# Kernel tuning notes

Hardware: AMD Instinct MI355X
Metric: run time of the kernel (lower is better)

The kernel has to match this reference:

```python
import jax, jax.numpy as jnp
import numpy as np
from jax import lax

B, C, H, W = 16, 256, 64, 64
HID = 128
EQ = 256


def _lstm_dir(x, Wih, Whh, b, hidden):
    # x: [N, T, D]; PyTorch gate order i, f, g, o
    N = x.shape[0]
    h0 = jnp.zeros((N, hidden), x.dtype)
    c0 = jnp.zeros((N, hidden), x.dtype)
    xT = jnp.swapaxes(x, 0, 1)  # [T, N, D]
    pre = jnp.einsum('tnd,gd->tng', xT, Wih) + b  # precompute input projection

    def step(carry, xt):
        h, c = carry
        g = xt + h @ Whh.T
        i, f, gg, o = jnp.split(g, 4, axis=-1)
        c = jax.nn.sigmoid(f) * c + jax.nn.sigmoid(i) * jnp.tanh(gg)
        h = jax.nn.sigmoid(o) * jnp.tanh(c)
        return (h, c), h

    _, hs = lax.scan(step, (h0, c0), pre)
    return jnp.swapaxes(hs, 0, 1)  # [N, T, hidden]


def _bilstm(x, Wih_f, Whh_f, b_f, Wih_b, Whh_b, b_b, hidden):
    hf = _lstm_dir(x, Wih_f, Whh_f, b_f, hidden)
    hb = _lstm_dir(x[:, ::-1], Wih_b, Whh_b, b_b, hidden)[:, ::-1]
    return jnp.concatenate([hf, hb], axis=-1)


def setup_inputs() -> dict:
    key = jax.random.key(0)
    ks = jax.random.split(key, 16)
    s = 1.0 / np.sqrt(HID)
    d = {}
    d['input'] = jax.random.normal(ks[0], (B, C, H, W), jnp.float32)
    # horizontal LSTM (input_size=C)
    d['h_Wih_f'] = jax.random.uniform(ks[1], (4 * HID, C), jnp.float32, -s, s)
    d['h_Whh_f'] = jax.random.uniform(ks[2], (4 * HID, HID), jnp.float32, -s, s)
    d['h_b_f'] = jax.random.uniform(ks[3], (4 * HID,), jnp.float32, -s, s)
    d['h_Wih_b'] = jax.random.uniform(ks[4], (4 * HID, C), jnp.float32, -s, s)
    d['h_Whh_b'] = jax.random.uniform(ks[5], (4 * HID, HID), jnp.float32, -s, s)
    d['h_b_b'] = jax.random.uniform(ks[6], (4 * HID,), jnp.float32, -s, s)
    # vertical LSTM (input_size=2*HID)
    d['v_Wih_f'] = jax.random.uniform(ks[7], (4 * HID, 2 * HID), jnp.float32, -s, s)
    d['v_Whh_f'] = jax.random.uniform(ks[8], (4 * HID, HID), jnp.float32, -s, s)
    d['v_b_f'] = jax.random.uniform(ks[9], (4 * HID,), jnp.float32, -s, s)
    d['v_Wih_b'] = jax.random.uniform(ks[10], (4 * HID, 2 * HID), jnp.float32, -s, s)
    d['v_Whh_b'] = jax.random.uniform(ks[11], (4 * HID, HID), jnp.float32, -s, s)
    d['v_b_b'] = jax.random.uniform(ks[12], (4 * HID,), jnp.float32, -s, s)
    # 1x1 convs (no bias)
    d['Wr'] = jax.random.normal(ks[13], (EQ, 2 * HID), jnp.float32) * 0.05
    d['Wl'] = jax.random.normal(ks[14], (EQ, C), jnp.float32) * 0.05
    d['alpha'] = jnp.zeros((1,), jnp.float32) + 0.5  # nonzero so output depends on attention
    return d


def reference(input, h_Wih_f, h_Whh_f, h_b_f, h_Wih_b, h_Whh_b, h_b_b,
              v_Wih_f, v_Whh_f, v_b_f, v_Wih_b, v_Whh_b, v_b_b, Wr, Wl, alpha):
    b, c, h, w = input.shape
    # transpose(1,3): [B, W, H, C]; horizontal LSTM runs over H for each w
    x = jnp.transpose(input, (0, 3, 2, 1))  # [B, W, H, C]
    xh = x.reshape(b * w, h, c)
    hor = _bilstm(xh, h_Wih_f, h_Whh_f, h_b_f, h_Wih_b, h_Whh_b, h_b_b, HID)
    hor = hor.reshape(b, w, h, 2 * HID)  # == torch horizontal_feature
    # vertical LSTM: sequences over W for each h-index
    xv = jnp.transpose(hor, (0, 2, 1, 3)).reshape(b * h, w, 2 * HID)
    ver = _bilstm(xv, v_Wih_f, v_Whh_f, v_b_f, v_Wih_b, v_Whh_b, v_b_b, HID)
    ver = ver.reshape(b, h, w, 2 * HID)  # vf[b, hi, wi, :]
    # torch: stack dim=2 -> [B, W, H, 2Hd]; permute(0,3,1,2) -> [B, 2Hd, W, H]
    vf = jnp.transpose(ver, (0, 3, 2, 1))  # [B, 2Hd, W, H]
    vf = jnp.einsum('oc,bcwh->bowh', Wr, vf)  # conv_right 1x1
    vf = vf.reshape(b, EQ, h * w)
    vf = jax.nn.softmax(vf, axis=2)
    # left branch
    q = jnp.einsum('oc,bchw->bohw', Wl, input)
    q_avg = jnp.mean(q, axis=(2, 3)).reshape(b, 1, EQ)
    q_avg = jax.nn.softmax(q_avg, axis=2)
    attention = jnp.matmul(q_avg, vf).reshape(b, 1, h, w)
    attention = jax.nn.sigmoid(attention)
    out = input * attention
    return out * alpha + input
```

## Files before the change

### kernel.cpp

```cpp
#include <hip/hip_runtime.h>
#include <hip/hip_bf16.h>

typedef unsigned short u16;
typedef unsigned int u32;
typedef unsigned char u8;
typedef __attribute__((ext_vector_type(8))) short s8v;
typedef __attribute__((ext_vector_type(4))) float f4v;

__device__ __forceinline__ float b2f(u16 u) {
  union { u32 i; float f; } v; v.i = ((u32)u) << 16; return v.f;
}
__device__ __forceinline__ u16 f2b(float f) {
  union { float f; u32 i; } v; v.f = f;
  u32 r = v.i + 0x7FFFu + ((v.i >> 16) & 1u);
  return (u16)(r >> 16);
}
__device__ __forceinline__ float rcpf(float x) { return __builtin_amdgcn_rcpf(x); }
__device__ __forceinline__ float ex2(float x) {
#if __has_builtin(__builtin_amdgcn_exp2f)
  return __builtin_amdgcn_exp2f(x);
#else
  return exp2f(x);
#endif
}
__device__ __forceinline__ float sigf(float x) { return rcpf(1.0f + __expf(-x)); }
template<bool HI>
__device__ __forceinline__ u32 pkfp8(float a, float b, u32 old) {
  return (u32)__builtin_amdgcn_cvt_pk_fp8_f32(a, b, (int)old, HI);
}

#define GS_IFO 1.4426950408889634f
#define GS_G   2.8853900817779268f

__device__ __forceinline__ void gl_lds16(const void* g, void* l) {
  __builtin_amdgcn_global_load_lds(
      (const __attribute__((address_space(1))) u32*)g,
      (__attribute__((address_space(3))) u32*)l, 16, 0, 0);
}

struct CvtArgs {
  const float* src[9];
  void* dst[9];
  int n4[9];
  int scl[9];
  int sh[9];
  int to8[9];
};
__global__ __launch_bounds__(256) void k_cvt(CvtArgs a) {
  int seg = blockIdx.y;
  int i = blockIdx.x * 256 + threadIdx.x;
  if (i >= a.n4[seg]) return;
  float4 v = ((const float4*)a.src[seg])[i];
  if (a.scl[seg]) {
    float s;
    if (a.scl[seg] == 2) {
      s = GS_IFO;
    } else {
      int r = i >> a.sh[seg];
      s = (((r >> 7) & 3) == 2) ? GS_G : GS_IFO;
    }
    v.x *= s; v.y *= s; v.z *= s; v.w *= s;
  }
  if (a.to8[seg]) {
    u32 p = pkfp8<false>(v.x, v.y, 0);
    p = pkfp8<true>(v.z, v.w, p);
    ((u32*)a.dst[seg])[i] = p;
  } else {
    ushort4 o;
    o.x = f2b(v.x); o.y = f2b(v.y); o.z = f2b(v.z); o.w = f2b(v.w);
    ((ushort4*)a.dst[seg])[i] = o;
  }
}

__global__ __launch_bounds__(256) void k_tin(const float* __restrict__ in,
                                             u8* __restrict__ A8,
                                             float* __restrict__ meansum) {
  int b = blockIdx.z, h = blockIdx.y, c0 = blockIdx.x * 64;
  int t = threadIdx.x, lane = t & 63, q = t >> 6;
  __shared__ u8 lT[64][68];
  const float* src = in + ((b * 256 + c0) * 64 + h) * 64;
#pragma unroll 4
  for (int i = 0; i < 16; ++i) {
    int cl = q * 16 + i;
    float v = src[cl * 4096 + lane];
    lT[cl][lane] = (u8)(pkfp8<false>(v, v, 0) & 0xffu);
    float s = v;
#pragma unroll
    for (int off = 32; off; off >>= 1) s += __shfl_xor(s, off);
    if (lane == 0) atomicAdd(&meansum[b * 256 + c0 + cl], s);
  }
  __syncthreads();
  u8* dst = A8 + (b * 4096 + h) * 256 + c0;
#pragma unroll 4
  for (int i = 0; i < 16; ++i) {
    int w = q * 16 + i;
    dst[w * 16384 + lane] = lT[lane][w];
  }
}

__global__ __launch_bounds__(256) void k_qavg(const float* __restrict__ meansum,
                                              const float* __restrict__ Wl,
                                              float* __restrict__ qavg) {
  int b = blockIdx.x, t = threadIdx.x;
  __shared__ float mean[256];
  __shared__ float red[256];
  mean[t] = meansum[b * 256 + t] * (1.0f / 4096.0f);
  __syncthreads();
  const float* wr = Wl + t * 256;
  float acc = 0.0f;
  for (int c = 0; c < 256; ++c) acc = fmaf(wr[c], mean[c], acc);
  red[t] = acc; __syncthreads();
  for (int s = 128; s; s >>= 1) { if (t < s) red[t] = fmaxf(red[t], red[t + s]); __syncthreads(); }
  float mx = red[0]; __syncthreads();
  float e = __expf(acc - mx);
  red[t] = e; __syncthreads();
  for (int s = 128; s; s >>= 1) { if (t < s) red[t] += red[t + s]; __syncthreads(); }
  qavg[b * 256 + t] = e / red[0];
}

__global__ __launch_bounds__(256, 4) void k_gemm2(const u16* __restrict__ A,
                                                  const u16* __restrict__ W,
                                                  u16* __restrict__ out, int nstride, int NT,
                                                  float* __restrict__ Zsum) {
  int nwg = gridDim.x;
  int q = nwg >> 3;
  int bid = blockIdx.x;
  int swz = (bid & 7) * q + (bid >> 3);
  int mt = swz / NT, nt = swz % NT;
  int mb = mt << 7, nb = nt << 7;
  int t = threadIdx.x, lane = t & 63, wid = t >> 6;
  int laneg = lane & 15, lk = lane >> 4;
  __shared__ __align__(16) u16 lA[128][64];
  __shared__ __align__(16) u16 lW[128][64];
  f4v acc[4][4] = {};
  int wm = wid >> 1, wn = wid & 1;
  for (int kb = 0; kb < 4; ++kb) {
    if (kb) __syncthreads();
#pragma unroll
    for (int k = 0; k < 4; ++k) {
      int rb = (wid << 5) + (k << 3);
      int r = rb + (lane >> 3);
      int cs = (lane & 7) ^ (r & 7);
      const u16* ga = A + (mb + r) * 256 + (kb << 6) + (cs << 3);
      const u16* gw = W + (nb + r) * 256 + (kb << 6) + (cs << 3);
      gl_lds16(ga, &lA[rb][0]);
      gl_lds16(gw, &lW[rb][0]);
    }
    __syncthreads();
#pragma unroll
    for (int kk = 0; kk < 2; ++kk) {
      s8v af[4], bf[4];
#pragma unroll
      for (int m = 0; m < 4; ++m) {
        int r = (wm << 6) + (m << 4) + laneg;
        int c = ((kk << 2) + lk) ^ (r & 7);
        af[m] = *(const s8v*)&lA[r][c << 3];
      }
#pragma unroll
      for (int n = 0; n < 4; ++n) {
        int r = (wn << 6) + (n << 4) + laneg;
        int c = ((kk << 2) + lk) ^ (r & 7);
        bf[n] = *(const s8v*)&lW[r][c << 3];
      }
#pragma unroll
      for (int m = 0; m < 4; ++m)
#pragma unroll
        for (int n = 0; n < 4; ++n)
          acc[m][n] = __builtin_amdgcn_mfma_f32_16x16x32_bf16(af[m], bf[n], acc[m][n], 0, 0, 0);
    }
  }
#pragma unroll
  for (int n = 0; n < 4; ++n) {
    int col = nb + (wn << 6) + (n << 4) + laneg;
    float csum = 0.f;
#pragma unroll
    for (int m = 0; m < 4; ++m) {
      int row0 = mb + (wm << 6) + (m << 4) + (lk << 2);
#pragma unroll
      for (int j = 0; j < 4; ++j) {
        float e = ex2(acc[m][n][j]);
        csum += e;
        out[(row0 + j) * nstride + col] = f2b(e);
      }
    }
    csum += __shfl_xor(csum, 16);
    csum += __shfl_xor(csum, 32);
    if (lk == 0) atomicAdd(&Zsum[((mb >> 12) << 8) + col], csum);
  }
}

template<bool OUT8>
__global__ __launch_bounds__(512, 1) void k_recur_f(const u8* __restrict__ X8,
                                                    const u8* __restrict__ Wi8,
                                                    const u16* __restrict__ Whh,
                                                    const float* __restrict__ bias_f,
                                                    const float* __restrict__ bias_b,
                                                    void* __restrict__ outp) {
  int dir = blockIdx.y;
  int s0 = blockIdx.x << 4;
  int t = threadIdx.x, lane = t & 63, w = t >> 6;
  int laneg = lane & 15, lk = lane >> 4;
  const u16* Wd = Whh + dir * 65536;
  const u8* Wi = Wi8 + dir * 131072;
  const float* bia = dir ? bias_b : bias_f;
  int hc = w << 4;
  s8v bfr[4][4];
#pragma unroll
  for (int g = 0; g < 4; ++g)
#pragma unroll
    for (int kk = 0; kk < 4; ++kk)
      bfr[g][kk] = *(const s8v*)(Wd + (g * 128 + hc + laneg) * 128 + kk * 32 + lk * 8);
  long long ifr[4][8];
#pragma unroll
  for (int g = 0; g < 4; ++g)
#pragma unroll
    for (int kk = 0; kk < 8; ++kk)
      ifr[g][kk] = *(const long long*)(Wi + (g * 128 + hc + laneg) * 256 + kk * 32 + lk * 8);
  float bval[4];
#pragma unroll
  for (int g = 0; g < 4; ++g)
    bval[g] = bia[g * 128 + hc + laneg] * ((g == 2) ? GS_G : GS_IFO);

  __shared__ __align__(16) u16 hb[2][16][136];
  __shared__ __align__(16) u8 xb[3][16][256];
  for (int i = t; i < 2 * 16 * 136; i += 512) ((u16*)hb)[i] = 0;

  float cs[4] = {0.f, 0.f, 0.f, 0.f};
  int tc0 = dir ? 63 : 0;
  int dstep = dir ? -1 : 1;
  int srw = (w << 2) + (lane >> 4);
  int c16 = lane & 15;
  const u8* xsrc = X8 + (s0 + srw) * 16384 + ((c16 ^ (srw & 7)) << 4);
  int srow = (w << 1) + (lane >> 5);
  int schunk = lane & 31;
  int rowb = ((s0 >> 6) << 12) + (s0 & 63);
  if (w < 4) {
    gl_lds16(xsrc + tc0 * 256, &xb[0][w << 2][0]);
    gl_lds16(xsrc + ((tc0 + dstep) & 63) * 256, &xb[1][w << 2][0]);
  }
  __syncthreads();
  int cur = 0;
  for (int st = 0; st < 64; ++st) {
    int tc = tc0 + st * dstep;
    if (st) {
      int pr = tc - dstep;
      uint2 hv = *(const uint2*)&hb[cur][srow][schunk << 2];
      if (OUT8) {
        float f0 = b2f((u16)(hv.x & 0xffff)), f1 = b2f((u16)(hv.x >> 16));
        float f2 = b2f((u16)(hv.y & 0xffff)), f3 = b2f((u16)(hv.y >> 16));
        u32 p = pkfp8<false>(f0, f1, 0);
        p = pkfp8<true>(f2, f3, p);
        *(u32*)((u8*)outp + (rowb + pr * 64 + srow) * 256 + (dir << 7) + (schunk << 2)) = p;
      } else {
        *(uint2*)((u16*)outp + (rowb + pr * 64 + srow) * 256 + (dir << 7) + (schunk << 2)) = hv;
      }
    }
    if (w < 4 && st < 62) {
      int tn = tc0 + (st + 2) * dstep;
      gl_lds16(xsrc + tn * 256, &xb[(st + 2) % 3][w << 2][0]);
    }
    f4v acc[4];
#pragma unroll
    for (int g = 0; g < 4; ++g)
      acc[g] = (f4v){bval[g], bval[g], bval[g], bval[g]};
    {
      const u8* xrow = &xb[st % 3][laneg][0];
      long long xf[8];
#pragma unroll
      for (int kk = 0; kk < 8; ++kk)
        xf[kk] = *(const long long*)&xrow[((((kk << 1) + (lk >> 1)) ^ (laneg & 7)) << 4) + ((lk & 1) << 3)];
#pragma unroll
      for (int g = 0; g < 4; ++g)
#pragma unroll
        for (int kk = 0; kk < 8; ++kk)
          acc[g] = __builtin_amdgcn_mfma_f32_16x16x32_fp8_fp8(xf[kk], ifr[g][kk], acc[g], 0, 0, 0);
    }
    {
      s8v afr[4];
#pragma unroll
      for (int kk = 0; kk < 4; ++kk)
        afr[kk] = *(const s8v*)&hb[cur][laneg][kk * 32 + lk * 8];
#pragma unroll
      for (int g = 0; g < 4; ++g)
#pragma unroll
        for (int kk = 0; kk < 4; ++kk)
          acc[g] = __builtin_amdgcn_mfma_f32_16x16x32_bf16(afr[kk], bfr[g][kk], acc[g], 0, 0, 0);
    }
    int nxt = cur ^ 1;
#pragma unroll
    for (int j = 0; j < 4; ++j) {
      float iv = rcpf(1.0f + ex2(-acc[0][j]));
      float fv = rcpf(1.0f + ex2(-acc[1][j]));
      float gv = 1.0f - 2.0f * rcpf(1.0f + ex2(acc[2][j]));
      float ov = rcpf(1.0f + ex2(-acc[3][j]));
      float c = fv * cs[j] + iv * gv;
      cs[j] = c;
      float th = 1.0f - 2.0f * rcpf(1.0f + ex2(c * GS_G));
      hb[nxt][lk * 4 + j][hc + laneg] = f2b(ov * th);
    }
    asm volatile("s_waitcnt lgkmcnt(0)" ::: "memory");
    __builtin_amdgcn_s_barrier();
    cur = nxt;
  }
  {
    int pr = tc0 + 63 * dstep;
    uint2 hv = *(const uint2*)&hb[cur][srow][schunk << 2];
    if (OUT8) {
      float f0 = b2f((u16)(hv.x & 0xffff)), f1 = b2f((u16)(hv.x >> 16));
      float f2 = b2f((u16)(hv.y & 0xffff)), f3 = b2f((u16)(hv.y >> 16));
      u32 p = pkfp8<false>(f0, f1, 0);
      p = pkfp8<true>(f2, f3, p);
      *(u32*)((u8*)outp + (rowb + pr * 64 + srow) * 256 + (dir << 7) + (schunk << 2)) = p;
    } else {
      *(uint2*)((u16*)outp + (rowb + pr * 64 + srow) * 256 + (dir << 7) + (schunk << 2)) = hv;
    }
  }
}

__global__ __launch_bounds__(256) void k_attfin(const u16* __restrict__ VF,
                                                const float* __restrict__ qavg,
                                                const float* __restrict__ Z,
                                                const float* __restrict__ in,
                                                const float* __restrict__ alpha,
                                                float* __restrict__ out) {
  int bx = blockIdx.x;
  int b = bx >> 6;
  int sp0 = (bx & 63) << 6;
  int t = threadIdx.x, lane = t & 63, wid = t >> 6;
  __shared__ __align__(16) float lwo[256];
  __shared__ float fac[64];
  lwo[t] = qavg[b * 256 + t] / Z[b * 256 + t];
  __syncthreads();
  float4 wo = *(const float4*)&lwo[lane * 4];
  int rowbase = b * 4096 + sp0;
#pragma unroll 4
  for (int i = 0; i < 16; ++i) {
    int r = wid * 16 + i;
    uint2 v = *(const uint2*)&VF[(rowbase + r) * 256 + lane * 4];
    float x0 = b2f((u16)(v.x & 0xffff)), x1 = b2f((u16)(v.x >> 16));
    float x2 = b2f((u16)(v.y & 0xffff)), x3 = b2f((u16)(v.y >> 16));
    float p = wo.x * x0 + wo.y * x1 + wo.z * x2 + wo.w * x3;
#pragma unroll
    for (int off = 32; off; off >>= 1) p += __shfl_xor(p, off);
    if (lane == 0) fac[r] = p;
  }
  __syncthreads();
  float al = alpha[0];
  if (t < 64) fac[t] = 1.0f + al * sigf(fac[t]);
  __syncthreads();
  int sp = t & 63;
  float f = fac[sp];
  const float* ip = in + (long)b * 1048576 + sp0 + sp;
  float* op = out + (long)b * 1048576 + sp0 + sp;
  int c0 = t >> 6;
#pragma unroll 8
  for (int c = c0; c < 256; c += 4) {
    op[c * 4096] = ip[c * 4096] * f;
  }
}

extern "C" void kernel_launch(void* const* d_in, const int* in_sizes, int n_in,
                              void* d_out, int out_size, void* d_ws, size_t ws_size,
                              hipStream_t stream) {
  const float* input   = (const float*)d_in[0];
  const float* h_Wih_f = (const float*)d_in[1];
  const float* h_Whh_f = (const float*)d_in[2];
  const float* h_b_f   = (const float*)d_in[3];
  const float* h_Wih_b = (const float*)d_in[4];
  const float* h_Whh_b = (const float*)d_in[5];
  const float* h_b_b   = (const float*)d_in[6];
  const float* v_Wih_f = (const float*)d_in[7];
  const float* v_Whh_f = (const float*)d_in[8];
  const float* v_b_f   = (const float*)d_in[9];
  const float* v_Wih_b = (const float*)d_in[10];
  const float* v_Whh_b = (const float*)d_in[11];
  const float* v_b_b   = (const float*)d_in[12];
  const float* Wr      = (const float*)d_in[13];
  const float* Wl      = (const float*)d_in[14];
  const float* alphap  = (const float*)d_in[15];

  char* ws = (char*)d_ws;
  u8*  Ah8   = (u8*)(ws + 0);
  u16* VF    = (u16*)(ws + 33554432);
  u8*  Wh8   = (u8*)(ws + 67108864);
  u8*  Wv8   = (u8*)(ws + 67371008);
  u16* WhhH  = (u16*)(ws + 67633152);
  u16* WhhV  = (u16*)(ws + 67895296);
  u16* Wrb   = (u16*)(ws + 68157440);
  float* meansum = (float*)(ws + 68288512);
  float* qavg    = (float*)(ws + 68304896);
  float* pZ      = (float*)(ws + 68321280);
  u8*  Av8 = (u8*)d_out;
  u16* Ar  = (u16*)(ws + 0);

  (void)hipMemsetAsync(meansum, 0, 16 * 256 * 4, stream);
  (void)hipMemsetAsync(pZ, 0, 16 * 256 * 4, stream);

  CvtArgs ca;
  ca.src[0] = h_Wih_f; ca.dst[0] = Wh8;           ca.n4[0] = 32768; ca.scl[0] = 1; ca.sh[0] = 6; ca.to8[0] = 1;
  ca.src[1] = h_Wih_b; ca.dst[1] = Wh8 + 131072;  ca.n4[1] = 32768; ca.scl[1] = 1; ca.sh[1] = 6; ca.to8[1] = 1;
  ca.src[2] = v_Wih_f; ca.dst[2] = Wv8;           ca.n4[2] = 32768; ca.scl[2] = 1; ca.sh[2] = 6; ca.to8[2] = 1;
  ca.src[3] = v_Wih_b; ca.dst[3] = Wv8 + 131072;  ca.n4[3] = 32768; ca.scl[3] = 1; ca.sh[3] = 6; ca.to8[3] = 1;
  ca.src[4] = h_Whh_f; ca.dst[4] = WhhH;          ca.n4[4] = 16384; ca.scl[4] = 1; ca.sh[4] = 5; ca.to8[4] = 0;
  ca.src[5] = h_Whh_b; ca.dst[5] = WhhH + 65536;  ca.n4[5] = 16384; ca.scl[5] = 1; ca.sh[5] = 5; ca.to8[5] = 0;
  ca.src[6] = v_Whh_f; ca.dst[6] = WhhV;          ca.n4[6] = 16384; ca.scl[6] = 1; ca.sh[6] = 5; ca.to8[6] = 0;
  ca.src[7] = v_Whh_b; ca.dst[7] = WhhV + 65536;  ca.n4[7] = 16384; ca.scl[7] = 1; ca.sh[7] = 5; ca.to8[7] = 0;
  ca.src[8] = Wr;      ca.dst[8] = Wrb;           ca.n4[8] = 16384; ca.scl[8] = 2; ca.sh[8] = 6; ca.to8[8] = 0;
  k_cvt<<<dim3(128, 9), 256, 0, stream>>>(ca);

  k_tin<<<dim3(4, 64, 16), 256, 0, stream>>>(input, Ah8, meansum);
  k_qavg<<<16, 256, 0, stream>>>(meansum, Wl, qavg);

  k_recur_f<true><<<dim3(64, 2), 512, 0, stream>>>(Ah8, Wh8, WhhH, h_b_f, h_b_b, (void*)Av8);
  k_recur_f<false><<<dim3(64, 2), 512, 0, stream>>>(Av8, Wv8, WhhV, v_b_f, v_b_b, (void*)Ar);
  k_gemm2<<<1024, 256, 0, stream>>>(Ar, Wrb, VF, 256, 2, pZ);

  k_attfin<<<1024, 256, 0, stream>>>(VF, qavg, pZ, input, alphap, (float*)d_out);
}
```

Measured before the change: 341.4 us.

## Switch recurrent weights, hidden state, and conv-right GEMM path to FP8

Converts the recurrent Whh weights and hidden-state LDS buffers from bf16 to fp8, so the recurrent step uses fp8 MFMA and writes outputs directly without repacking. The 1x1 conv GEMM now takes fp8 inputs, loads the whole K=256 tile into LDS in one pass, and stores exp values as fp8, which halves the intermediate traffic read by the attention-final kernel. The aim is to cut LDS and HBM bandwidth and shorten the serial recurrence, at the cost of lower numerical precision in the hidden state and softmax numerators. The two memsets are merged into one.

```diff
diff --git a/kernel.cpp b/kernel.cpp
--- a/kernel.cpp
+++ b/kernel.cpp
@@ -4,6 +4,7 @@
 typedef unsigned short u16;
 typedef unsigned int u32;
 typedef unsigned char u8;
+typedef long long ll8;
 typedef __attribute__((ext_vector_type(8))) short s8v;
 typedef __attribute__((ext_vector_type(4))) float f4v;
 
@@ -28,6 +29,20 @@
 __device__ __forceinline__ u32 pkfp8(float a, float b, u32 old) {
   return (u32)__builtin_amdgcn_cvt_pk_fp8_f32(a, b, (int)old, HI);
 }
+__device__ __forceinline__ u8 f2f8(float x) { return (u8)(pkfp8<false>(x, x, 0) & 0xffu); }
+template<int S>
+__device__ __forceinline__ float f8tof(u32 v) {
+#if __has_builtin(__builtin_amdgcn_cvt_f32_fp8)
+  return __builtin_amdgcn_cvt_f32_fp8((int)v, S);
+#else
+  u8 b = (u8)(v >> (8 * S));
+  u32 s = (b >> 7) & 1u, e = (b >> 3) & 15u, m = b & 7u;
+  union { u32 i; float f; } r;
+  if (e) r.i = (s << 31) | ((e + 120u) << 23) | (m << 20);
+  else { r.f = (float)m * 0.001953125f; r.i |= s << 31; }
+  return r.f;
+#endif
+}
 
 #define GS_IFO 1.4426950408889634f
 #define GS_G   2.8853900817779268f
@@ -40,36 +55,27 @@
 
 struct CvtArgs {
   const float* src[9];
-  void* dst[9];
+  u8* dst[9];
   int n4[9];
   int scl[9];
   int sh[9];
-  int to8[9];
 };
 __global__ __launch_bounds__(256) void k_cvt(CvtArgs a) {
   int seg = blockIdx.y;
   int i = blockIdx.x * 256 + threadIdx.x;
   if (i >= a.n4[seg]) return;
   float4 v = ((const float4*)a.src[seg])[i];
-  if (a.scl[seg]) {
-    float s;
-    if (a.scl[seg] == 2) {
-      s = GS_IFO;
-    } else {
-      int r = i >> a.sh[seg];
-      s = (((r >> 7) & 3) == 2) ? GS_G : GS_IFO;
-    }
-    v.x *= s; v.y *= s; v.z *= s; v.w *= s;
-  }
-  if (a.to8[seg]) {
-    u32 p = pkfp8<false>(v.x, v.y, 0);
-    p = pkfp8<true>(v.z, v.w, p);
-    ((u32*)a.dst[seg])[i] = p;
+  float s;
+  if (a.scl[seg] == 2) {
+    s = GS_IFO;
   } else {
-    ushort4 o;
-    o.x = f2b(v.x); o.y = f2b(v.y); o.z = f2b(v.z); o.w = f2b(v.w);
-    ((ushort4*)a.dst[seg])[i] = o;
-  }
+    int r = i >> a.sh[seg];
+    s = (((r >> 7) & 3) == 2) ? GS_G : GS_IFO;
+  }
+  v.x *= s; v.y *= s; v.z *= s; v.w *= s;
+  u32 p = pkfp8<false>(v.x, v.y, 0);
+  p = pkfp8<true>(v.z, v.w, p);
+  ((u32*)a.dst[seg])[i] = p;
 }
 
 __global__ __launch_bounds__(256) void k_tin(const float* __restrict__ in,
@@ -83,7 +89,7 @@
   for (int i = 0; i < 16; ++i) {
     int cl = q * 16 + i;
     float v = src[cl * 4096 + lane];
-    lT[cl][lane] = (u8)(pkfp8<false>(v, v, 0) & 0xffu);
+    lT[cl][lane] = f2f8(v);
     float s = v;
 #pragma unroll
     for (int off = 32; off; off >>= 1) s += __shfl_xor(s, off);
@@ -118,56 +124,55 @@
   qavg[b * 256 + t] = e / red[0];
 }
 
-__global__ __launch_bounds__(256, 4) void k_gemm2(const u16* __restrict__ A,
-                                                  const u16* __restrict__ W,
-                                                  u16* __restrict__ out, int nstride, int NT,
+__global__ __launch_bounds__(256, 2) void k_gemm8(const u8* __restrict__ A,
+                                                  const u8* __restrict__ W,
+                                                  u8* __restrict__ out,
                                                   float* __restrict__ Zsum) {
   int nwg = gridDim.x;
   int q = nwg >> 3;
   int bid = blockIdx.x;
   int swz = (bid & 7) * q + (bid >> 3);
-  int mt = swz / NT, nt = swz % NT;
+  int mt = swz >> 1, nt = swz & 1;
   int mb = mt << 7, nb = nt << 7;
   int t = threadIdx.x, lane = t & 63, wid = t >> 6;
   int laneg = lane & 15, lk = lane >> 4;
-  __shared__ __align__(16) u16 lA[128][64];
-  __shared__ __align__(16) u16 lW[128][64];
+  __shared__ __align__(16) u8 lA[128][256];
+  __shared__ __align__(16) u8 lW[128][256];
+  {
+    int rl = lane >> 4;
+    int unit = lane & 15;
+#pragma unroll
+    for (int i = 0; i < 8; ++i) {
+      int rb4 = ((wid << 3) + i) << 2;
+      int r = rb4 + rl;
+      int usA = unit ^ (r & 7);
+      gl_lds16(A + (mb + r) * 256 + (usA << 4), &lA[rb4][0]);
+      gl_lds16(W + (nb + r) * 256 + (usA << 4), &lW[rb4][0]);
+    }
+  }
+  __syncthreads();
   f4v acc[4][4] = {};
   int wm = wid >> 1, wn = wid & 1;
-  for (int kb = 0; kb < 4; ++kb) {
-    if (kb) __syncthreads();
-#pragma unroll
-    for (int k = 0; k < 4; ++k) {
-      int rb = (wid << 5) + (k << 3);
-      int r = rb + (lane >> 3);
-      int cs = (lane & 7) ^ (r & 7);
-      const u16* ga = A + (mb + r) * 256 + (kb << 6) + (cs << 3);
-      const u16* gw = W + (nb + r) * 256 + (kb << 6) + (cs << 3);
-      gl_lds16(ga, &lA[rb][0]);
-      gl_lds16(gw, &lW[rb][0]);
-    }
-    __syncthreads();
-#pragma unroll
-    for (int kk = 0; kk < 2; ++kk) {
-      s8v af[4], bf[4];
-#pragma unroll
-      for (int m = 0; m < 4; ++m) {
-        int r = (wm << 6) + (m << 4) + laneg;
-        int c = ((kk << 2) + lk) ^ (r & 7);
-        af[m] = *(const s8v*)&lA[r][c << 3];
-      }
-#pragma unroll
-      for (int n = 0; n < 4; ++n) {
-        int r = (wn << 6) + (n << 4) + laneg;
-        int c = ((kk << 2) + lk) ^ (r & 7);
-        bf[n] = *(const s8v*)&lW[r][c << 3];
-      }
-#pragma unroll
-      for (int m = 0; m < 4; ++m)
-#pragma unroll
-        for (int n = 0; n < 4; ++n)
-          acc[m][n] = __builtin_amdgcn_mfma_f32_16x16x32_bf16(af[m], bf[n], acc[m][n], 0, 0, 0);
-    }
+#pragma unroll
+  for (int kk = 0; kk < 8; ++kk) {
+    ll8 af[4], bf[4];
+#pragma unroll
+    for (int m = 0; m < 4; ++m) {
+      int r = (wm << 6) + (m << 4) + laneg;
+      int us = ((kk << 1) + (lk >> 1)) ^ (r & 7);
+      af[m] = *(const ll8*)&lA[r][(us << 4) + ((lk & 1) << 3)];
+    }
+#pragma unroll
+    for (int n = 0; n < 4; ++n) {
+      int r = (wn << 6) + (n << 4) + laneg;
+      int us = ((kk << 1) + (lk >> 1)) ^ (r & 7);
+      bf[n] = *(const ll8*)&lW[r][(us << 4) + ((lk & 1) << 3)];
+    }
+#pragma unroll
+    for (int m = 0; m < 4; ++m)
+#pragma unroll
+      for (int n = 0; n < 4; ++n)
+        acc[m][n] = __builtin_amdgcn_mfma_f32_16x16x32_fp8_fp8(af[m], bf[n], acc[m][n], 0, 0, 0);
   }
 #pragma unroll
   for (int n = 0; n < 4; ++n) {
@@ -180,7 +185,7 @@
       for (int j = 0; j < 4; ++j) {
         float e = ex2(acc[m][n][j]);
         csum += e;
-        out[(row0 + j) * nstride + col] = f2b(e);
+        out[(row0 + j) * 256 + col] = f2f8(e);
       }
     }
     csum += __shfl_xor(csum, 16);
@@ -189,41 +194,40 @@
   }
 }
 
-template<bool OUT8>
 __global__ __launch_bounds__(512, 1) void k_recur_f(const u8* __restrict__ X8,
                                                     const u8* __restrict__ Wi8,
-                                                    const u16* __restrict__ Whh,
+                                                    const u8* __restrict__ Wh8d,
                                                     const float* __restrict__ bias_f,
                                                     const float* __restrict__ bias_b,
-                                                    void* __restrict__ outp) {
+                                                    u8* __restrict__ outb) {
   int dir = blockIdx.y;
   int s0 = blockIdx.x << 4;
   int t = threadIdx.x, lane = t & 63, w = t >> 6;
   int laneg = lane & 15, lk = lane >> 4;
-  const u16* Wd = Whh + dir * 65536;
+  const u8* Wd = Wh8d + dir * 65536;
   const u8* Wi = Wi8 + dir * 131072;
   const float* bia = dir ? bias_b : bias_f;
   int hc = w << 4;
-  s8v bfr[4][4];
+  ll8 bfr[4][4];
 #pragma unroll
   for (int g = 0; g < 4; ++g)
 #pragma unroll
     for (int kk = 0; kk < 4; ++kk)
-      bfr[g][kk] = *(const s8v*)(Wd + (g * 128 + hc + laneg) * 128 + kk * 32 + lk * 8);
-  long long ifr[4][8];
+      bfr[g][kk] = *(const ll8*)(Wd + (g * 128 + hc + laneg) * 128 + kk * 32 + lk * 8);
+  ll8 ifr[4][8];
 #pragma unroll
   for (int g = 0; g < 4; ++g)
 #pragma unroll
     for (int kk = 0; kk < 8; ++kk)
-      ifr[g][kk] = *(const long long*)(Wi + (g * 128 + hc + laneg) * 256 + kk * 32 + lk * 8);
+      ifr[g][kk] = *(const ll8*)(Wi + (g * 128 + hc + laneg) * 256 + kk * 32 + lk * 8);
   float bval[4];
 #pragma unroll
   for (int g = 0; g < 4; ++g)
     bval[g] = bia[g * 128 + hc + laneg] * ((g == 2) ? GS_G : GS_IFO);
 
-  __shared__ __align__(16) u16 hb[2][16][136];
+  __shared__ __align__(16) u8 hb[2][16][144];
   __shared__ __align__(16) u8 xb[3][16][256];
-  for (int i = t; i < 2 * 16 * 136; i += 512) ((u16*)hb)[i] = 0;
+  for (int i = t; i < 2 * 16 * 144; i += 512) ((u8*)hb)[i] = 0;
 
   float cs[4] = {0.f, 0.f, 0.f, 0.f};
   int tc0 = dir ? 63 : 0;
@@ -231,8 +235,8 @@
   int srw = (w << 2) + (lane >> 4);
   int c16 = lane & 15;
   const u8* xsrc = X8 + (s0 + srw) * 16384 + ((c16 ^ (srw & 7)) << 4);
-  int srow = (w << 1) + (lane >> 5);
-  int schunk = lane & 31;
+  int srow = t >> 5;
+  int schunk = t & 31;
   int rowb = ((s0 >> 6) << 12) + (s0 & 63);
   if (w < 4) {
     gl_lds16(xsrc + tc0 * 256, &xb[0][w << 2][0]);
@@ -244,16 +248,8 @@
     int tc = tc0 + st * dstep;
     if (st) {
       int pr = tc - dstep;
-      uint2 hv = *(const uint2*)&hb[cur][srow][schunk << 2];
-      if (OUT8) {
-        float f0 = b2f((u16)(hv.x & 0xffff)), f1 = b2f((u16)(hv.x >> 16));
-        float f2 = b2f((u16)(hv.y & 0xffff)), f3 = b2f((u16)(hv.y >> 16));
-        u32 p = pkfp8<false>(f0, f1, 0);
-        p = pkfp8<true>(f2, f3, p);
-        *(u32*)((u8*)outp + (rowb + pr * 64 + srow) * 256 + (dir << 7) + (schunk << 2)) = p;
-      } else {
-        *(uint2*)((u16*)outp + (rowb + pr * 64 + srow) * 256 + (dir << 7) + (schunk << 2)) = hv;
-      }
+      u32 hv = *(const u32*)&hb[cur][srow][schunk << 2];
+      *(u32*)(outb + (rowb + pr * 64 + srow) * 256 + (dir << 7) + (schunk << 2)) = hv;
     }
     if (w < 4 && st < 62) {
       int tn = tc0 + (st + 2) * dstep;
@@ -265,10 +261,10 @@
       acc[g] = (f4v){bval[g], bval[g], bval[g], bval[g]};
     {
       const u8* xrow = &xb[st % 3][laneg][0];
-      long long xf[8];
+      ll8 xf[8];
 #pragma unroll
       for (int kk = 0; kk < 8; ++kk)
-        xf[kk] = *(const long long*)&xrow[((((kk << 1) + (lk >> 1)) ^ (laneg & 7)) << 4) + ((lk & 1) << 3)];
+        xf[kk] = *(const ll8*)&xrow[((((kk << 1) + (lk >> 1)) ^ (laneg & 7)) << 4) + ((lk & 1) << 3)];
 #pragma unroll
       for (int g = 0; g < 4; ++g)
 #pragma unroll
@@ -276,15 +272,15 @@
           acc[g] = __builtin_amdgcn_mfma_f32_16x16x32_fp8_fp8(xf[kk], ifr[g][kk], acc[g], 0, 0, 0);
     }
     {
-      s8v afr[4];
+      ll8 afr[4];
 #pragma unroll
       for (int kk = 0; kk < 4; ++kk)
-        afr[kk] = *(const s8v*)&hb[cur][laneg][kk * 32 + lk * 8];
+        afr[kk] = *(const ll8*)&hb[cur][laneg][kk * 32 + lk * 8];
 #pragma unroll
       for (int g = 0; g < 4; ++g)
 #pragma unroll
         for (int kk = 0; kk < 4; ++kk)
-          acc[g] = __builtin_amdgcn_mfma_f32_16x16x32_bf16(afr[kk], bfr[g][kk], acc[g], 0, 0, 0);
+          acc[g] = __builtin_amdgcn_mfma_f32_16x16x32_fp8_fp8(afr[kk], bfr[g][kk], acc[g], 0, 0, 0);
     }
     int nxt = cur ^ 1;
 #pragma unroll
@@ -296,7 +292,7 @@
       float c = fv * cs[j] + iv * gv;
       cs[j] = c;
       float th = 1.0f - 2.0f * rcpf(1.0f + ex2(c * GS_G));
-      hb[nxt][lk * 4 + j][hc + laneg] = f2b(ov * th);
+      hb[nxt][(lk << 2) + j][hc + laneg] = f2f8(ov * th);
     }
     asm volatile("s_waitcnt lgkmcnt(0)" ::: "memory");
     __builtin_amdgcn_s_barrier();
@@ -304,20 +300,12 @@
   }
   {
     int pr = tc0 + 63 * dstep;
-    uint2 hv = *(const uint2*)&hb[cur][srow][schunk << 2];
-    if (OUT8) {
-      float f0 = b2f((u16)(hv.x & 0xffff)), f1 = b2f((u16)(hv.x >> 16));
-      float f2 = b2f((u16)(hv.y & 0xffff)), f3 = b2f((u16)(hv.y >> 16));
-      u32 p = pkfp8<false>(f0, f1, 0);
-      p = pkfp8<true>(f2, f3, p);
-      *(u32*)((u8*)outp + (rowb + pr * 64 + srow) * 256 + (dir << 7) + (schunk << 2)) = p;
-    } else {
-      *(uint2*)((u16*)outp + (rowb + pr * 64 + srow) * 256 + (dir << 7) + (schunk << 2)) = hv;
-    }
-  }
-}
-
-__global__ __launch_bounds__(256) void k_attfin(const u16* __restrict__ VF,
+    u32 hv = *(const u32*)&hb[cur][srow][schunk << 2];
+    *(u32*)(outb + (rowb + pr * 64 + srow) * 256 + (dir << 7) + (schunk << 2)) = hv;
+  }
+}
+
+__global__ __launch_bounds__(256) void k_attfin(const u8* __restrict__ VF8,
                                                 const float* __restrict__ qavg,
                                                 const float* __restrict__ Z,
                                                 const float* __restrict__ in,
@@ -336,10 +324,9 @@
 #pragma unroll 4
   for (int i = 0; i < 16; ++i) {
     int r = wid * 16 + i;
-    uint2 v = *(const uint2*)&VF[(rowbase + r) * 256 + lane * 4];
-    float x0 = b2f((u16)(v.x & 0xffff)), x1 = b2f((u16)(v.x >> 16));
-    float x2 = b2f((u16)(v.y & 0xffff)), x3 = b2f((u16)(v.y >> 16));
-    float p = wo.x * x0 + wo.y * x1 + wo.z * x2 + wo.w * x3;
+    u32 v = *(const u32*)&VF8[(rowbase + r) * 256 + lane * 4];
+    float p = wo.x * f8tof<0>(v) + wo.y * f8tof<1>(v) +
+              wo.z * f8tof<2>(v) + wo.w * f8tof<3>(v);
 #pragma unroll
     for (int off = 32; off; off >>= 1) p += __shfl_xor(p, off);
     if (lane == 0) fac[r] = p;
@@ -381,39 +368,38 @@
 
   char* ws = (char*)d_ws;
   u8*  Ah8   = (u8*)(ws + 0);
-  u16* VF    = (u16*)(ws + 33554432);
+  u8*  VF8   = (u8*)(ws + 33554432);
   u8*  Wh8   = (u8*)(ws + 67108864);
   u8*  Wv8   = (u8*)(ws + 67371008);
-  u16* WhhH  = (u16*)(ws + 67633152);
-  u16* WhhV  = (u16*)(ws + 67895296);
-  u16* Wrb   = (u16*)(ws + 68157440);
-  float* meansum = (float*)(ws + 68288512);
-  float* qavg    = (float*)(ws + 68304896);
-  float* pZ      = (float*)(ws + 68321280);
+  u8*  WhhH8 = (u8*)(ws + 67633152);
+  u8*  WhhV8 = (u8*)(ws + 67764224);
+  u8*  Wrb8  = (u8*)(ws + 67895296);
+  float* meansum = (float*)(ws + 67960832);
+  float* qavg    = (float*)(ws + 67977216);
+  float* pZ      = (float*)(ws + 67993600);
   u8*  Av8 = (u8*)d_out;
-  u16* Ar  = (u16*)(ws + 0);
-
-  (void)hipMemsetAsync(meansum, 0, 16 * 256 * 4, stream);
-  (void)hipMemsetAsync(pZ, 0, 16 * 256 * 4, stream);
+  u8*  Ar8 = Ah8;
+
+  (void)hipMemsetAsync(meansum, 0, 3 * 16384, stream);
 
   CvtArgs ca;
-  ca.src[0] = h_Wih_f; ca.dst[0] = Wh8;           ca.n4[0] = 32768; ca.scl[0] = 1; ca.sh[0] = 6; ca.to8[0] = 1;
-  ca.src[1] = h_Wih_b; ca.dst[1] = Wh8 + 131072;  ca.n4[1] = 32768; ca.scl[1] = 1; ca.sh[1] = 6; ca.to8[1] = 1;
-  ca.src[2] = v_Wih_f; ca.dst[2] = Wv8;           ca.n4[2] = 32768; ca.scl[2] = 1; ca.sh[2] = 6; ca.to8[2] = 1;
-  ca.src[3] = v_Wih_b; ca.dst[3] = Wv8 + 131072;  ca.n4[3] = 32768; ca.scl[3] = 1; ca.sh[3] = 6; ca.to8[3] = 1;
-  ca.src[4] = h_Whh_f; ca.dst[4] = WhhH;          ca.n4[4] = 16384; ca.scl[4] = 1; ca.sh[4] = 5; ca.to8[4] = 0;
-  ca.src[5] = h_Whh_b; ca.dst[5] = WhhH + 65536;  ca.n4[5] = 16384; ca.scl[5] = 1; ca.sh[5] = 5; ca.to8[5] = 0;
-  ca.src[6] = v_Whh_f; ca.dst[6] = WhhV;          ca.n4[6] = 16384; ca.scl[6] = 1; ca.sh[6] = 5; ca.to8[6] = 0;
-  ca.src[7] = v_Whh_b; ca.dst[7] = WhhV + 65536;  ca.n4[7] = 16384; ca.scl[7] = 1; ca.sh[7] = 5; ca.to8[7] = 0;
-  ca.src[8] = Wr;      ca.dst[8] = Wrb;           ca.n4[8] = 16384; ca.scl[8] = 2; ca.sh[8] = 6; ca.to8[8] = 0;
+  ca.src[0] = h_Wih_f; ca.dst[0] = Wh8;           ca.n4[0] = 32768; ca.scl[0] = 1; ca.sh[0] = 6;
+  ca.src[1] = h_Wih_b; ca.dst[1] = Wh8 + 131072;  ca.n4[1] = 32768; ca.scl[1] = 1; ca.sh[1] = 6;
+  ca.src[2] = v_Wih_f; ca.dst[2] = Wv8;           ca.n4[2] = 32768; ca.scl[2] = 1; ca.sh[2] = 6;
+  ca.src[3] = v_Wih_b; ca.dst[3] = Wv8 + 131072;  ca.n4[3] = 32768; ca.scl[3] = 1; ca.sh[3] = 6;
+  ca.src[4] = h_Whh_f; ca.dst[4] = WhhH8;         ca.n4[4] = 16384; ca.scl[4] = 1; ca.sh[4] = 5;
+  ca.src[5] = h_Whh_b; ca.dst[5] = WhhH8 + 65536; ca.n4[5] = 16384; ca.scl[5] = 1; ca.sh[5] = 5;
+  ca.src[6] = v_Whh_f; ca.dst[6] = WhhV8;         ca.n4[6] = 16384; ca.scl[6] = 1; ca.sh[6] = 5;
+  ca.src[7] = v_Whh_b; ca.dst[7] = WhhV8 + 65536; ca.n4[7] = 16384; ca.scl[7] = 1; ca.sh[7] = 5;
+  ca.src[8] = Wr;      ca.dst[8] = Wrb8;          ca.n4[8] = 16384; ca.scl[8] = 2; ca.sh[8] = 6;
   k_cvt<<<dim3(128, 9), 256, 0, stream>>>(ca);
 
   k_tin<<<dim3(4, 64, 16), 256, 0, stream>>>(input, Ah8, meansum);
   k_qavg<<<16, 256, 0, stream>>>(meansum, Wl, qavg);
 
-  k_recur_f<true><<<dim3(64, 2), 512, 0, stream>>>(Ah8, Wh8, WhhH, h_b_f, h_b_b, (void*)Av8);
-  k_recur_f<false><<<dim3(64, 2), 512, 0, stream>>>(Av8, Wv8, WhhV, v_b_f, v_b_b, (void*)Ar);
-  k_gemm2<<<1024, 256, 0, stream>>>(Ar, Wrb, VF, 256, 2, pZ);
-
-  k_attfin<<<1024, 256, 0, stream>>>(VF, qavg, pZ, input, alphap, (float*)d_out);
-}
+  k_recur_f<<<dim3(64, 2), 512, 0, stream>>>(Ah8, Wh8, WhhH8, h_b_f, h_b_b, Av8);
+  k_recur_f<<<dim3(64, 2), 512, 0, stream>>>(Av8, Wv8, WhhV8, v_b_f, v_b_b, Ar8);
+  k_gemm8<<<1024, 256, 0, stream>>>(Ar8, Wrb8, VF8, pZ);
+
+  k_attfin<<<1024, 256, 0, stream>>>(VF8, qavg, pZ, input, alphap, (float*)d_out);
+}
```

New measurement: 315.6 us. 7.5% less time.
